# Kernel optimization log

Hardware: AMD Instinct MI355X
Metric: run time of the kernel (lower is better)

The kernel has to match this reference:

```python
import jax, jax.numpy as jnp
import numpy as np

B, N, F = 256, 32, 256
NUM_PASSING = 2


def _fc_edges(n):
    # all ordered pairs (send -> rec), i != j, matching NRI-style encode matrices
    send, rec = [], []
    for i in range(n):
        for j in range(n):
            if i != j:
                send.append(i)
                rec.append(j)
    return np.array(send, np.int32), np.array(rec, np.int32)


def setup_inputs() -> dict:
    key = jax.random.key(0)
    ks = jax.random.split(key, 16)
    send_np, rec_np = _fc_edges(N)

    def xavier(k, shape):
        fan_in, fan_out = shape
        std = (2.0 / (fan_in + fan_out)) ** 0.5
        return jax.random.normal(k, shape, jnp.float32) * std

    bias = lambda d: jnp.full((d,), 0.1, jnp.float32)
    return {
        "x": jax.random.normal(ks[0], (B, N, F), jnp.float32),
        "rec_idx": jnp.asarray(rec_np),
        "send_idx": jnp.asarray(send_np),
        "w_in1": xavier(ks[1], (F, 256)), "b_in1": bias(256),
        "w_in2": xavier(ks[2], (256, 256)), "b_in2": bias(256),
        "w_e1": xavier(ks[3], (512, 256)), "b_e1": bias(256),
        "w_e2": xavier(ks[4], (256, 256)), "b_e2": bias(256),
        "w_n1": xavier(ks[5], (256, 256)), "b_n1": bias(256),
        "w_n2": xavier(ks[6], (256, 256)), "b_n2": bias(256),
    }


def _mlp(h, wa, ba, wb, bb):
    # Linear -> ReLU -> (Dropout p=0) -> Linear -> ReLU
    return jax.nn.relu(jax.nn.relu(h @ wa + ba) @ wb + bb)


def reference(x, rec_idx, send_idx,
              w_in1, b_in1, w_in2, b_in2,
              w_e1, b_e1, w_e2, b_e2,
              w_n1, b_n1, w_n2, b_n2):
    n_nodes = x.shape[-2]
    # in-degree per node == rec_encode.sum(0)
    deg = jax.ops.segment_sum(jnp.ones_like(rec_idx, x.dtype), rec_idx,
                              num_segments=n_nodes)  # [N]
    h = _mlp(x, w_in1, b_in1, w_in2, b_in2)  # [B, N, 256]
    for _ in range(NUM_PASSING):
        # node2edge: gather (== one-hot matmul), cat [sends, recs]
        edges = jnp.concatenate([h[:, send_idx, :], h[:, rec_idx, :]], axis=-1)  # [B, E, 512]
        e = _mlp(edges, w_e1, b_e1, w_e2, b_e2)  # [B, E, 256]
        # edge2node: scatter-sum by receiver then divide by in-degree (mean)
        e_t = jnp.swapaxes(e, 0, 1)  # [E, B, 256]
        agg = jax.ops.segment_sum(e_t, rec_idx, num_segments=n_nodes)  # [N, B, 256]
        agg = jnp.swapaxes(agg, 0, 1) / deg[None, :, None]  # [B, N, 256]
        h = _mlp(agg, w_n1, b_n1, w_n2, b_n2)
    return h
```

## Files before the change

### kernel.cpp

```cpp
#include <hip/hip_runtime.h>


typedef short bf16x8 __attribute__((ext_vector_type(8)));
typedef float f32x4 __attribute__((ext_vector_type(4)));
typedef unsigned short ushort_t;

__device__ __forceinline__ unsigned short f2bf(float f) {
    unsigned u = __float_as_uint(f);
    u += 0x7fff + ((u >> 16) & 1);
    return (unsigned short)(u >> 16);
}
__device__ __forceinline__ float lo16f(unsigned w) { return __uint_as_float(w << 16); }
__device__ __forceinline__ float hi16f(unsigned w) { return __uint_as_float(w & 0xffff0000u); }
__device__ __forceinline__ unsigned cvt_pk_bf16(float lo, float hi) {
    unsigned r;
    asm volatile("v_cvt_pk_bf16_f32 %0, %1, %2" : "=v"(r) : "v"(lo), "v"(hi));
    return r;
}
__device__ __forceinline__ void gload16(const void* g, void* l) {
    __builtin_amdgcn_global_load_lds(
        (const __attribute__((address_space(1))) void*)g,
        (__attribute__((address_space(3))) void*)l, 16, 0, 0);
}

__global__ __launch_bounds__(256) void prep_weights(
    const float* __restrict__ w_in1, const float* __restrict__ w_in2,
    const float* __restrict__ w_e1,  const float* __restrict__ w_e2,
    const float* __restrict__ w_n1,  const float* __restrict__ w_n2,
    ushort_t* __restrict__ dst)
{
    __shared__ ushort_t tile[32][264];
    const int wid = blockIdx.x >> 3;
    const int kb  = blockIdx.x & 7;
    const float* src;
    switch (wid) {
        case 0: src = w_in1; break;
        case 1: src = w_in2; break;
        case 2: src = w_e1; break;
        case 3: src = w_e1 + 65536; break;
        case 4: src = w_e2; break;
        case 5: src = w_n1; break;
        default: src = w_n2; break;
    }
    const int t = threadIdx.x;
#pragma unroll
    for (int k0 = 0; k0 < 32; k0++)
        tile[k0][t] = f2bf(src[(size_t)(kb * 32 + k0) * 256 + t]);
    __syncthreads();
    ushort_t* base = dst + wid * 65536 + kb * 8192 + t * 32;
    const int sw = (t >> 1) & 3;
#pragma unroll
    for (int kc = 0; kc < 4; kc++) {
        union { uint4 q; ushort_t u[8]; } w;
#pragma unroll
        for (int ko = 0; ko < 8; ko++) w.u[ko] = tile[kc * 8 + ko][t];
        *(uint4*)&base[(kc ^ sw) * 8] = w.q;
    }
}

__global__ __launch_bounds__(256) void conv_x(
    const float* __restrict__ x, ushort_t* __restrict__ xb, int n8)
{
    int i = blockIdx.x * 256 + threadIdx.x;
    if (i >= n8) return;
    const float4* p = (const float4*)x + (size_t)i * 2;
    float4 a = p[0], b = p[1];
    ushort4 o0 = make_ushort4(f2bf(a.x), f2bf(a.y), f2bf(a.z), f2bf(a.w));
    ushort4 o1 = make_ushort4(f2bf(b.x), f2bf(b.y), f2bf(b.z), f2bf(b.w));
    ((ushort4*)xb)[(size_t)i * 2]     = o0;
    ((ushort4*)xb)[(size_t)i * 2 + 1] = o1;
}

template <int EPI>
__global__ __launch_bounds__(256) void gemm64(
    const ushort_t* __restrict__ A, const ushort_t* __restrict__ WB,
    const float* __restrict__ bias, void* __restrict__ out, int ldc, int split)
{
    __shared__ ushort_t As[2][2048];
    __shared__ ushort_t Bs[2][2048];

    const int mb = (blockIdx.x & 7) * 16 + (blockIdx.x >> 3);
    const int m0 = mb * 64;
    const int ny = blockIdx.y;
    int nloc; const ushort_t* wb; const float* bp; int nout;
    if (ny >= split) { nloc = (ny - split) * 64; wb = WB + 65536; bp = nullptr; nout = 256 + nloc; }
    else             { nloc = ny * 64;           wb = WB;         bp = bias;    nout = nloc; }

    const int t = threadIdx.x;
    const int lane = t & 63;
    const int w = t >> 6;
    const int wm = w >> 1, wn = w & 1;
    const int lr = lane & 15, lg = lane >> 4;

    const int arow = w * 16 + (lane >> 2);
    const int ac = (lane & 3) ^ ((arow >> 1) & 3);
    const ushort_t* asrc = A + (size_t)(m0 + arow) * 256 + ac * 8;
    const ushort_t* bsrc = wb + nloc * 32 + w * 512 + lane * 8;

    int aoff[2], boff[2];
#pragma unroll
    for (int f = 0; f < 2; f++) {
        int r = wm * 32 + f * 16 + lr;
        aoff[f] = r * 32 + ((lg ^ ((r >> 1) & 3)) * 8);
        int rb = wn * 32 + f * 16 + lr;
        boff[f] = rb * 32 + ((lg ^ ((rb >> 1) & 3)) * 8);
    }

    f32x4 acc[2][2] = {};

    gload16(asrc, &As[0][w * 512]);
    gload16(bsrc, &Bs[0][w * 512]);

    for (int kb = 1; kb < 8; kb++) {
        __syncthreads();
        gload16(asrc + kb * 32,   &As[kb & 1][w * 512]);
        gload16(bsrc + kb * 8192, &Bs[kb & 1][w * 512]);
        const int cur = (kb - 1) & 1;
        bf16x8 a0 = *(const bf16x8*)&As[cur][aoff[0]];
        bf16x8 a1 = *(const bf16x8*)&As[cur][aoff[1]];
        bf16x8 b0 = *(const bf16x8*)&Bs[cur][boff[0]];
        bf16x8 b1 = *(const bf16x8*)&Bs[cur][boff[1]];
        acc[0][0] = __builtin_amdgcn_mfma_f32_16x16x32_bf16(a0, b0, acc[0][0], 0, 0, 0);
        acc[0][1] = __builtin_amdgcn_mfma_f32_16x16x32_bf16(a0, b1, acc[0][1], 0, 0, 0);
        acc[1][0] = __builtin_amdgcn_mfma_f32_16x16x32_bf16(a1, b0, acc[1][0], 0, 0, 0);
        acc[1][1] = __builtin_amdgcn_mfma_f32_16x16x32_bf16(a1, b1, acc[1][1], 0, 0, 0);
    }
    __syncthreads();
    {
        bf16x8 a0 = *(const bf16x8*)&As[1][aoff[0]];
        bf16x8 a1 = *(const bf16x8*)&As[1][aoff[1]];
        bf16x8 b0 = *(const bf16x8*)&Bs[1][boff[0]];
        bf16x8 b1 = *(const bf16x8*)&Bs[1][boff[1]];
        acc[0][0] = __builtin_amdgcn_mfma_f32_16x16x32_bf16(a0, b0, acc[0][0], 0, 0, 0);
        acc[0][1] = __builtin_amdgcn_mfma_f32_16x16x32_bf16(a0, b1, acc[0][1], 0, 0, 0);
        acc[1][0] = __builtin_amdgcn_mfma_f32_16x16x32_bf16(a1, b0, acc[1][0], 0, 0, 0);
        acc[1][1] = __builtin_amdgcn_mfma_f32_16x16x32_bf16(a1, b1, acc[1][1], 0, 0, 0);
    }

#pragma unroll
    for (int fm = 0; fm < 2; fm++)
#pragma unroll
        for (int fn = 0; fn < 2; fn++) {
            const int cl = wn * 32 + fn * 16 + lr;
            float bv = 0.f;
            if (bp) bv = bp[nloc + cl];
#pragma unroll
            for (int r = 0; r < 4; r++) {
                const int row = m0 + wm * 32 + fm * 16 + lg * 4 + r;
                float v = acc[fm][fn][r] + bv;
                if constexpr (EPI == 2 || EPI == 3) v = fmaxf(v, 0.f);
                if constexpr (EPI == 3)
                    ((float*)out)[(size_t)row * ldc + nout + cl] = v;
                else
                    ((ushort_t*)out)[(size_t)row * ldc + nout + cl] = f2bf(v);
            }
        }
}

__global__ __launch_bounds__(256, 2) void edge_fused(
    const ushort_t* __restrict__ UVb,
    const ushort_t* __restrict__ WBsw,
    const float* __restrict__ b2,
    ushort_t* __restrict__ agg)
{
    __shared__ ushort_t As[2][4096];

    const int logical = (blockIdx.x & 7) * 256 + (blockIdx.x >> 3);
    const int bb = logical >> 3;
    const int g0 = (logical & 7) * 4;
    const int t = threadIdx.x;
    const int lane = t & 63;
    const int w = t >> 6;
    const int lr = lane & 15, lg = lane >> 4;

    const int brow = t >> 1;
    const int kh = t & 1;
    const int jr = brow >> 5;
    const int s = brow & 31;
    const int j = g0 + jr;
    const int si = (s == 31) ? j : (s + (s >= j ? 1 : 0));
    const ushort_t* up = UVb + (size_t)(bb * 32 + si) * 512 + kh * 16;
    const ushort_t* vp = UVb + (size_t)(bb * 32 + j) * 512 + 256 + kh * 16;
    const int swz = (brow >> 1) & 3;
    const int aw0 = brow * 32 + (((kh * 2)     ^ swz) * 8);
    const int aw1 = brow * 32 + (((kh * 2 + 1) ^ swz) * 8);

    int aoff[8];
#pragma unroll
    for (int m = 0; m < 8; m++) {
        const int r = m * 16 + lr;
        aoff[m] = r * 32 + ((lg ^ ((r >> 1) & 3)) * 8);
    }
    int boff[4];
#pragma unroll
    for (int fn = 0; fn < 4; fn++) {
        const int n = w * 64 + fn * 16 + lr;
        boff[fn] = n * 32 + ((lg ^ ((n >> 1) & 3)) * 8);
    }

    {
        uint4 ua = *(const uint4*)up,        ub = *(const uint4*)(up + 8);
        uint4 va = *(const uint4*)vp,        vb = *(const uint4*)(vp + 8);
        uint4 q0, q1;
        q0.x = cvt_pk_bf16(fmaxf(lo16f(ua.x) + lo16f(va.x), 0.f), fmaxf(hi16f(ua.x) + hi16f(va.x), 0.f));
        q0.y = cvt_pk_bf16(fmaxf(lo16f(ua.y) + lo16f(va.y), 0.f), fmaxf(hi16f(ua.y) + hi16f(va.y), 0.f));
        q0.z = cvt_pk_bf16(fmaxf(lo16f(ua.z) + lo16f(va.z), 0.f), fmaxf(hi16f(ua.z) + hi16f(va.z), 0.f));
        q0.w = cvt_pk_bf16(fmaxf(lo16f(ua.w) + lo16f(va.w), 0.f), fmaxf(hi16f(ua.w) + hi16f(va.w), 0.f));
        q1.x = cvt_pk_bf16(fmaxf(lo16f(ub.x) + lo16f(vb.x), 0.f), fmaxf(hi16f(ub.x) + hi16f(vb.x), 0.f));
        q1.y = cvt_pk_bf16(fmaxf(lo16f(ub.y) + lo16f(vb.y), 0.f), fmaxf(hi16f(ub.y) + hi16f(vb.y), 0.f));
        q1.z = cvt_pk_bf16(fmaxf(lo16f(ub.z) + lo16f(vb.z), 0.f), fmaxf(hi16f(ub.z) + hi16f(vb.z), 0.f));
        q1.w = cvt_pk_bf16(fmaxf(lo16f(ub.w) + lo16f(vb.w), 0.f), fmaxf(hi16f(ub.w) + hi16f(vb.w), 0.f));
        *(uint4*)&As[0][aw0] = q0;
        *(uint4*)&As[0][aw1] = q1;
    }
    bf16x8 bc[4];
#pragma unroll
    for (int fn = 0; fn < 4; fn++) bc[fn] = *(const bf16x8*)&WBsw[boff[fn]];

    f32x4 acc[8][4] = {};

#pragma unroll
    for (int kb = 0; kb < 8; kb++) {
        __syncthreads();
        uint4 ua, ub, va, vb;
        bf16x8 bn[4];
        if (kb < 7) {
            const ushort_t* upn = up + (kb + 1) * 32;
            const ushort_t* vpn = vp + (kb + 1) * 32;
            ua = *(const uint4*)upn;  ub = *(const uint4*)(upn + 8);
            va = *(const uint4*)vpn;  vb = *(const uint4*)(vpn + 8);
#pragma unroll
            for (int fn = 0; fn < 4; fn++)
                bn[fn] = *(const bf16x8*)&WBsw[(kb + 1) * 8192 + boff[fn]];
        }
        bf16x8 af[8];
#pragma unroll
        for (int m = 0; m < 8; m++) af[m] = *(const bf16x8*)&As[kb & 1][aoff[m]];
#pragma unroll
        for (int fn = 0; fn < 4; fn++)
#pragma unroll
            for (int m = 0; m < 8; m++)
                acc[m][fn] = __builtin_amdgcn_mfma_f32_16x16x32_bf16(
                    af[m], bc[fn], acc[m][fn], 0, 0, 0);
        if (kb < 7) {
            uint4 q0, q1;
            q0.x = cvt_pk_bf16(fmaxf(lo16f(ua.x) + lo16f(va.x), 0.f), fmaxf(hi16f(ua.x) + hi16f(va.x), 0.f));
            q0.y = cvt_pk_bf16(fmaxf(lo16f(ua.y) + lo16f(va.y), 0.f), fmaxf(hi16f(ua.y) + hi16f(va.y), 0.f));
            q0.z = cvt_pk_bf16(fmaxf(lo16f(ua.z) + lo16f(va.z), 0.f), fmaxf(hi16f(ua.z) + hi16f(va.z), 0.f));
            q0.w = cvt_pk_bf16(fmaxf(lo16f(ua.w) + lo16f(va.w), 0.f), fmaxf(hi16f(ua.w) + hi16f(va.w), 0.f));
            q1.x = cvt_pk_bf16(fmaxf(lo16f(ub.x) + lo16f(vb.x), 0.f), fmaxf(hi16f(ub.x) + hi16f(vb.x), 0.f));
            q1.y = cvt_pk_bf16(fmaxf(lo16f(ub.y) + lo16f(vb.y), 0.f), fmaxf(hi16f(ub.y) + hi16f(vb.y), 0.f));
            q1.z = cvt_pk_bf16(fmaxf(lo16f(ub.z) + lo16f(vb.z), 0.f), fmaxf(hi16f(ub.z) + hi16f(vb.z), 0.f));
            q1.w = cvt_pk_bf16(fmaxf(lo16f(ub.w) + lo16f(vb.w), 0.f), fmaxf(hi16f(ub.w) + hi16f(vb.w), 0.f));
            *(uint4*)&As[(kb + 1) & 1][aw0] = q0;
            *(uint4*)&As[(kb + 1) & 1][aw1] = q1;
#pragma unroll
            for (int fn = 0; fn < 4; fn++) bc[fn] = bn[fn];
        }
    }

#pragma unroll
    for (int fn = 0; fn < 4; fn++) {
        const int col = w * 64 + fn * 16 + lr;
        const float bvf = b2[col];
#pragma unroll
        for (int recv = 0; recv < 4; recv++) {
            float sum = 0.f;
#pragma unroll
            for (int q = 0; q < 2; q++) {
                const int fm = recv * 2 + q;
#pragma unroll
                for (int r = 0; r < 4; r++) {
                    float v = fmaxf(acc[fm][fn][r] + bvf, 0.f);
                    if (!(q == 1 && lg == 3 && r == 3)) sum += v;
                }
            }
            sum += __shfl_xor(sum, 16);
            sum += __shfl_xor(sum, 32);
            if (lane < 16)
                agg[(size_t)(bb * 32 + g0 + recv) * 256 + col] = f2bf(sum * (1.0f / 31.0f));
        }
    }
}

extern "C" void kernel_launch(void* const* d_in, const int* in_sizes, int n_in,
                              void* d_out, int out_size, void* d_ws, size_t ws_size,
                              hipStream_t stream)
{
    const float* x     = (const float*)d_in[0];
    const float* w_in1 = (const float*)d_in[3];
    const float* b_in1 = (const float*)d_in[4];
    const float* w_in2 = (const float*)d_in[5];
    const float* b_in2 = (const float*)d_in[6];
    const float* w_e1  = (const float*)d_in[7];
    const float* b_e1  = (const float*)d_in[8];
    const float* w_e2  = (const float*)d_in[9];
    const float* b_e2  = (const float*)d_in[10];
    const float* w_n1  = (const float*)d_in[11];
    const float* b_n1  = (const float*)d_in[12];
    const float* w_n2  = (const float*)d_in[13];
    const float* b_n2  = (const float*)d_in[14];

    char* ws = (char*)d_ws;
    size_t off = 0;
    auto alloc = [&](size_t n) { char* p = ws + off; off += (n + 255) & ~(size_t)255; return p; };

    ushort_t* wt  = (ushort_t*)alloc(7 * 65536 * sizeof(ushort_t));
    ushort_t* xb  = (ushort_t*)alloc(8192 * 256 * 2);
    ushort_t* h   = (ushort_t*)alloc(8192 * 256 * 2);
    ushort_t* t1  = (ushort_t*)alloc(8192 * 256 * 2);
    ushort_t* UVb = (ushort_t*)alloc(8192 * 512 * 2);
    ushort_t* ag  = (ushort_t*)alloc(8192 * 256 * 2);
    (void)ws_size; (void)in_sizes; (void)n_in; (void)out_size;

    prep_weights<<<56, 256, 0, stream>>>(w_in1, w_in2, w_e1, w_e2, w_n1, w_n2, wt);
    conv_x<<<1024, 256, 0, stream>>>(x, xb, 262144);

    dim3 gs(128, 4);
    gemm64<2><<<gs, 256, 0, stream>>>(xb, wt + 0 * 65536, b_in1, t1, 256, 99);
    gemm64<2><<<gs, 256, 0, stream>>>(t1, wt + 1 * 65536, b_in2, h, 256, 99);

    for (int p = 0; p < 2; p++) {
        dim3 guv(128, 8);
        gemm64<4><<<guv, 256, 0, stream>>>(h, wt + 2 * 65536, b_e1, UVb, 512, 4);
        edge_fused<<<2048, 256, 0, stream>>>(UVb, wt + 4 * 65536, b_e2, ag);
        gemm64<2><<<gs, 256, 0, stream>>>(ag, wt + 5 * 65536, b_n1, t1, 256, 99);
        if (p == 0)
            gemm64<2><<<gs, 256, 0, stream>>>(t1, wt + 6 * 65536, b_n2, h, 256, 99);
        else
            gemm64<3><<<gs, 256, 0, stream>>>(t1, wt + 6 * 65536, b_n2, (float*)d_out, 256, 99);
    }
}
```

Baseline: 146.4 us.

## Stage full-K A tiles in LDS and stream B from global in GEMMs

```diff
diff --git a/kernel.cpp b/kernel.cpp
--- a/kernel.cpp
+++ b/kernel.cpp
@@ -72,15 +72,14 @@
 }
 
 template <int EPI>
-__global__ __launch_bounds__(256) void gemm64(
+__global__ __launch_bounds__(256, 2) void gemm128(
     const ushort_t* __restrict__ A, const ushort_t* __restrict__ WB,
     const float* __restrict__ bias, void* __restrict__ out, int ldc, int split)
 {
-    __shared__ ushort_t As[2][2048];
-    __shared__ ushort_t Bs[2][2048];
-
-    const int mb = (blockIdx.x & 7) * 16 + (blockIdx.x >> 3);
-    const int m0 = mb * 64;
+    __shared__ ushort_t As[128 * 256];
+
+    const int mb = (blockIdx.x & 7) * 8 + (blockIdx.x >> 3);
+    const int m0 = mb * 128;
     const int ny = blockIdx.y;
     int nloc; const ushort_t* wb; const float* bp; int nout;
     if (ny >= split) { nloc = (ny - split) * 64; wb = WB + 65536; bp = nullptr; nout = 256 + nloc; }
@@ -89,70 +88,76 @@
     const int t = threadIdx.x;
     const int lane = t & 63;
     const int w = t >> 6;
-    const int wm = w >> 1, wn = w & 1;
     const int lr = lane & 15, lg = lane >> 4;
 
-    const int arow = w * 16 + (lane >> 2);
-    const int ac = (lane & 3) ^ ((arow >> 1) & 3);
-    const ushort_t* asrc = A + (size_t)(m0 + arow) * 256 + ac * 8;
-    const ushort_t* bsrc = wb + nloc * 32 + w * 512 + lane * 8;
-
-    int aoff[2], boff[2];
-#pragma unroll
-    for (int f = 0; f < 2; f++) {
-        int r = wm * 32 + f * 16 + lr;
-        aoff[f] = r * 32 + ((lg ^ ((r >> 1) & 3)) * 8);
-        int rb = wn * 32 + f * 16 + lr;
-        boff[f] = rb * 32 + ((lg ^ ((rb >> 1) & 3)) * 8);
-    }
-
-    f32x4 acc[2][2] = {};
-
-    gload16(asrc, &As[0][w * 512]);
-    gload16(bsrc, &Bs[0][w * 512]);
-
-    for (int kb = 1; kb < 8; kb++) {
-        __syncthreads();
-        gload16(asrc + kb * 32,   &As[kb & 1][w * 512]);
-        gload16(bsrc + kb * 8192, &Bs[kb & 1][w * 512]);
-        const int cur = (kb - 1) & 1;
-        bf16x8 a0 = *(const bf16x8*)&As[cur][aoff[0]];
-        bf16x8 a1 = *(const bf16x8*)&As[cur][aoff[1]];
-        bf16x8 b0 = *(const bf16x8*)&Bs[cur][boff[0]];
-        bf16x8 b1 = *(const bf16x8*)&Bs[cur][boff[1]];
-        acc[0][0] = __builtin_amdgcn_mfma_f32_16x16x32_bf16(a0, b0, acc[0][0], 0, 0, 0);
-        acc[0][1] = __builtin_amdgcn_mfma_f32_16x16x32_bf16(a0, b1, acc[0][1], 0, 0, 0);
-        acc[1][0] = __builtin_amdgcn_mfma_f32_16x16x32_bf16(a1, b0, acc[1][0], 0, 0, 0);
-        acc[1][1] = __builtin_amdgcn_mfma_f32_16x16x32_bf16(a1, b1, acc[1][1], 0, 0, 0);
-    }
+    {
+        const int r0  = w * 2 + (lane >> 5);
+        const int kcp = lane & 31;
+        const ushort_t* src = A + (size_t)(m0 + r0) * 256 + ((kcp ^ (r0 & 7)) * 8);
+        ushort_t* dst = &As[w * 512];
+#pragma unroll
+        for (int i = 0; i < 16; i++)
+            gload16(src + i * 2048, dst + i * 2048);
+    }
+
+    int boffs[4]; float bv[4];
+#pragma unroll
+    for (int fn = 0; fn < 4; fn++) {
+        const int n = nloc + fn * 16 + lr;
+        boffs[fn] = n * 32 + ((lg ^ ((n >> 1) & 3)) * 8);
+        bv[fn] = bp ? bp[n] : 0.f;
+    }
+    int abase[2], asw[2];
+#pragma unroll
+    for (int fm = 0; fm < 2; fm++) {
+        const int r = w * 32 + fm * 16 + lr;
+        abase[fm] = r * 256;
+        asw[fm] = r & 7;
+    }
+
+    bf16x8 bc[4];
+#pragma unroll
+    for (int fn = 0; fn < 4; fn++) bc[fn] = *(const bf16x8*)&wb[boffs[fn]];
+
     __syncthreads();
-    {
-        bf16x8 a0 = *(const bf16x8*)&As[1][aoff[0]];
-        bf16x8 a1 = *(const bf16x8*)&As[1][aoff[1]];
-        bf16x8 b0 = *(const bf16x8*)&Bs[1][boff[0]];
-        bf16x8 b1 = *(const bf16x8*)&Bs[1][boff[1]];
-        acc[0][0] = __builtin_amdgcn_mfma_f32_16x16x32_bf16(a0, b0, acc[0][0], 0, 0, 0);
-        acc[0][1] = __builtin_amdgcn_mfma_f32_16x16x32_bf16(a0, b1, acc[0][1], 0, 0, 0);
-        acc[1][0] = __builtin_amdgcn_mfma_f32_16x16x32_bf16(a1, b0, acc[1][0], 0, 0, 0);
-        acc[1][1] = __builtin_amdgcn_mfma_f32_16x16x32_bf16(a1, b1, acc[1][1], 0, 0, 0);
+
+    f32x4 acc[2][4] = {};
+#pragma unroll
+    for (int kb = 0; kb < 8; kb++) {
+        bf16x8 bn[4];
+        if (kb < 7)
+#pragma unroll
+            for (int fn = 0; fn < 4; fn++)
+                bn[fn] = *(const bf16x8*)&wb[(kb + 1) * 8192 + boffs[fn]];
+        bf16x8 af[2];
+#pragma unroll
+        for (int fm = 0; fm < 2; fm++)
+            af[fm] = *(const bf16x8*)&As[abase[fm] + (((kb * 4 + lg) ^ asw[fm]) * 8)];
+#pragma unroll
+        for (int fm = 0; fm < 2; fm++)
+#pragma unroll
+            for (int fn = 0; fn < 4; fn++)
+                acc[fm][fn] = __builtin_amdgcn_mfma_f32_16x16x32_bf16(
+                    af[fm], bc[fn], acc[fm][fn], 0, 0, 0);
+        if (kb < 7)
+#pragma unroll
+            for (int fn = 0; fn < 4; fn++) bc[fn] = bn[fn];
     }
 
 #pragma unroll
     for (int fm = 0; fm < 2; fm++)
 #pragma unroll
-        for (int fn = 0; fn < 2; fn++) {
-            const int cl = wn * 32 + fn * 16 + lr;
-            float bv = 0.f;
-            if (bp) bv = bp[nloc + cl];
+        for (int fn = 0; fn < 4; fn++) {
+            const int col = nout + fn * 16 + lr;
 #pragma unroll
             for (int r = 0; r < 4; r++) {
-                const int row = m0 + wm * 32 + fm * 16 + lg * 4 + r;
-                float v = acc[fm][fn][r] + bv;
+                const int row = m0 + w * 32 + fm * 16 + lg * 4 + r;
+                float v = acc[fm][fn][r] + bv[fn];
                 if constexpr (EPI == 2 || EPI == 3) v = fmaxf(v, 0.f);
                 if constexpr (EPI == 3)
-                    ((float*)out)[(size_t)row * ldc + nout + cl] = v;
+                    ((float*)out)[(size_t)row * ldc + col] = v;
                 else
-                    ((ushort_t*)out)[(size_t)row * ldc + nout + cl] = f2bf(v);
+                    ((ushort_t*)out)[(size_t)row * ldc + col] = f2bf(v);
             }
         }
 }
@@ -163,7 +168,7 @@
     const float* __restrict__ b2,
     ushort_t* __restrict__ agg)
 {
-    __shared__ ushort_t As[2][4096];
+    __shared__ ushort_t As[128 * 256];
 
     const int logical = (blockIdx.x & 7) * 256 + (blockIdx.x >> 3);
     const int bb = logical >> 3;
@@ -173,96 +178,77 @@
     const int w = t >> 6;
     const int lr = lane & 15, lg = lane >> 4;
 
-    const int brow = t >> 1;
-    const int kh = t & 1;
-    const int jr = brow >> 5;
-    const int s = brow & 31;
-    const int j = g0 + jr;
+    const int br = t >> 1;
+    const int h  = t & 1;
+    const int jr = br >> 5;
+    const int s  = br & 31;
+    const int j  = g0 + jr;
     const int si = (s == 31) ? j : (s + (s >= j ? 1 : 0));
-    const ushort_t* up = UVb + (size_t)(bb * 32 + si) * 512 + kh * 16;
-    const ushort_t* vp = UVb + (size_t)(bb * 32 + j) * 512 + 256 + kh * 16;
-    const int swz = (brow >> 1) & 3;
-    const int aw0 = brow * 32 + (((kh * 2)     ^ swz) * 8);
-    const int aw1 = brow * 32 + (((kh * 2 + 1) ^ swz) * 8);
-
-    int aoff[8];
+    const ushort_t* up = UVb + (size_t)(bb * 32 + si) * 512 + h * 128;
+    const ushort_t* vp = UVb + (size_t)(bb * 32 + j) * 512 + 256 + h * 128;
+    ushort_t* aw = &As[br * 256];
+    const int bsw = br & 7;
+
+#pragma unroll
+    for (int i = 0; i < 16; i++) {
+        uint4 u = *(const uint4*)(up + i * 8);
+        uint4 v = *(const uint4*)(vp + i * 8);
+        uint4 q;
+        q.x = cvt_pk_bf16(fmaxf(lo16f(u.x) + lo16f(v.x), 0.f), fmaxf(hi16f(u.x) + hi16f(v.x), 0.f));
+        q.y = cvt_pk_bf16(fmaxf(lo16f(u.y) + lo16f(v.y), 0.f), fmaxf(hi16f(u.y) + hi16f(v.y), 0.f));
+        q.z = cvt_pk_bf16(fmaxf(lo16f(u.z) + lo16f(v.z), 0.f), fmaxf(hi16f(u.z) + hi16f(v.z), 0.f));
+        q.w = cvt_pk_bf16(fmaxf(lo16f(u.w) + lo16f(v.w), 0.f), fmaxf(hi16f(u.w) + hi16f(v.w), 0.f));
+        *(uint4*)&aw[((h * 16 + i) ^ bsw) * 8] = q;
+    }
+
+    int abase[8], asw[8];
 #pragma unroll
     for (int m = 0; m < 8; m++) {
         const int r = m * 16 + lr;
-        aoff[m] = r * 32 + ((lg ^ ((r >> 1) & 3)) * 8);
-    }
-    int boff[4];
+        abase[m] = r * 256;
+        asw[m] = r & 7;
+    }
+    int boffs[4]; float bv[4];
 #pragma unroll
     for (int fn = 0; fn < 4; fn++) {
         const int n = w * 64 + fn * 16 + lr;
-        boff[fn] = n * 32 + ((lg ^ ((n >> 1) & 3)) * 8);
-    }
-
-    {
-        uint4 ua = *(const uint4*)up,        ub = *(const uint4*)(up + 8);
-        uint4 va = *(const uint4*)vp,        vb = *(const uint4*)(vp + 8);
-        uint4 q0, q1;
-        q0.x = cvt_pk_bf16(fmaxf(lo16f(ua.x) + lo16f(va.x), 0.f), fmaxf(hi16f(ua.x) + hi16f(va.x), 0.f));
-        q0.y = cvt_pk_bf16(fmaxf(lo16f(ua.y) + lo16f(va.y), 0.f), fmaxf(hi16f(ua.y) + hi16f(va.y), 0.f));
-        q0.z = cvt_pk_bf16(fmaxf(lo16f(ua.z) + lo16f(va.z), 0.f), fmaxf(hi16f(ua.z) + hi16f(va.z), 0.f));
-        q0.w = cvt_pk_bf16(fmaxf(lo16f(ua.w) + lo16f(va.w), 0.f), fmaxf(hi16f(ua.w) + hi16f(va.w), 0.f));
-        q1.x = cvt_pk_bf16(fmaxf(lo16f(ub.x) + lo16f(vb.x), 0.f), fmaxf(hi16f(ub.x) + hi16f(vb.x), 0.f));
-        q1.y = cvt_pk_bf16(fmaxf(lo16f(ub.y) + lo16f(vb.y), 0.f), fmaxf(hi16f(ub.y) + hi16f(vb.y), 0.f));
-        q1.z = cvt_pk_bf16(fmaxf(lo16f(ub.z) + lo16f(vb.z), 0.f), fmaxf(hi16f(ub.z) + hi16f(vb.z), 0.f));
-        q1.w = cvt_pk_bf16(fmaxf(lo16f(ub.w) + lo16f(vb.w), 0.f), fmaxf(hi16f(ub.w) + hi16f(vb.w), 0.f));
-        *(uint4*)&As[0][aw0] = q0;
-        *(uint4*)&As[0][aw1] = q1;
+        boffs[fn] = n * 32 + ((lg ^ ((n >> 1) & 3)) * 8);
+        bv[fn] = b2[n];
     }
     bf16x8 bc[4];
 #pragma unroll
-    for (int fn = 0; fn < 4; fn++) bc[fn] = *(const bf16x8*)&WBsw[boff[fn]];
+    for (int fn = 0; fn < 4; fn++) bc[fn] = *(const bf16x8*)&WBsw[boffs[fn]];
+
+    __syncthreads();
 
     f32x4 acc[8][4] = {};
-
 #pragma unroll
     for (int kb = 0; kb < 8; kb++) {
-        __syncthreads();
-        uint4 ua, ub, va, vb;
         bf16x8 bn[4];
-        if (kb < 7) {
-            const ushort_t* upn = up + (kb + 1) * 32;
-            const ushort_t* vpn = vp + (kb + 1) * 32;
-            ua = *(const uint4*)upn;  ub = *(const uint4*)(upn + 8);
-            va = *(const uint4*)vpn;  vb = *(const uint4*)(vpn + 8);
+        if (kb < 7)
 #pragma unroll
             for (int fn = 0; fn < 4; fn++)
-                bn[fn] = *(const bf16x8*)&WBsw[(kb + 1) * 8192 + boff[fn]];
-        }
+                bn[fn] = *(const bf16x8*)&WBsw[(kb + 1) * 8192 + boffs[fn]];
         bf16x8 af[8];
 #pragma unroll
-        for (int m = 0; m < 8; m++) af[m] = *(const bf16x8*)&As[kb & 1][aoff[m]];
+        for (int m = 0; m < 8; m++)
+            af[m] = *(const bf16x8*)&As[abase[m] + (((kb * 4 + lg) ^ asw[m]) * 8)];
+        __builtin_amdgcn_s_setprio(1);
 #pragma unroll
         for (int fn = 0; fn < 4; fn++)
 #pragma unroll
             for (int m = 0; m < 8; m++)
                 acc[m][fn] = __builtin_amdgcn_mfma_f32_16x16x32_bf16(
                     af[m], bc[fn], acc[m][fn], 0, 0, 0);
-        if (kb < 7) {
-            uint4 q0, q1;
-            q0.x = cvt_pk_bf16(fmaxf(lo16f(ua.x) + lo16f(va.x), 0.f), fmaxf(hi16f(ua.x) + hi16f(va.x), 0.f));
-            q0.y = cvt_pk_bf16(fmaxf(lo16f(ua.y) + lo16f(va.y), 0.f), fmaxf(hi16f(ua.y) + hi16f(va.y), 0.f));
-            q0.z = cvt_pk_bf16(fmaxf(lo16f(ua.z) + lo16f(va.z), 0.f), fmaxf(hi16f(ua.z) + hi16f(va.z), 0.f));
-            q0.w = cvt_pk_bf16(fmaxf(lo16f(ua.w) + lo16f(va.w), 0.f), fmaxf(hi16f(ua.w) + hi16f(va.w), 0.f));
-            q1.x = cvt_pk_bf16(fmaxf(lo16f(ub.x) + lo16f(vb.x), 0.f), fmaxf(hi16f(ub.x) + hi16f(vb.x), 0.f));
-            q1.y = cvt_pk_bf16(fmaxf(lo16f(ub.y) + lo16f(vb.y), 0.f), fmaxf(hi16f(ub.y) + hi16f(vb.y), 0.f));
-            q1.z = cvt_pk_bf16(fmaxf(lo16f(ub.z) + lo16f(vb.z), 0.f), fmaxf(hi16f(ub.z) + hi16f(vb.z), 0.f));
-            q1.w = cvt_pk_bf16(fmaxf(lo16f(ub.w) + lo16f(vb.w), 0.f), fmaxf(hi16f(ub.w) + hi16f(vb.w), 0.f));
-            *(uint4*)&As[(kb + 1) & 1][aw0] = q0;
-            *(uint4*)&As[(kb + 1) & 1][aw1] = q1;
+        __builtin_amdgcn_s_setprio(0);
+        if (kb < 7)
 #pragma unroll
             for (int fn = 0; fn < 4; fn++) bc[fn] = bn[fn];
-        }
     }
 
 #pragma unroll
     for (int fn = 0; fn < 4; fn++) {
         const int col = w * 64 + fn * 16 + lr;
-        const float bvf = b2[col];
 #pragma unroll
         for (int recv = 0; recv < 4; recv++) {
             float sum = 0.f;
@@ -271,7 +257,7 @@
                 const int fm = recv * 2 + q;
 #pragma unroll
                 for (int r = 0; r < 4; r++) {
-                    float v = fmaxf(acc[fm][fn][r] + bvf, 0.f);
+                    float v = fmaxf(acc[fm][fn][r] + bv[fn], 0.f);
                     if (!(q == 1 && lg == 3 && r == 3)) sum += v;
                 }
             }
@@ -316,18 +302,18 @@
     prep_weights<<<56, 256, 0, stream>>>(w_in1, w_in2, w_e1, w_e2, w_n1, w_n2, wt);
     conv_x<<<1024, 256, 0, stream>>>(x, xb, 262144);
 
-    dim3 gs(128, 4);
-    gemm64<2><<<gs, 256, 0, stream>>>(xb, wt + 0 * 65536, b_in1, t1, 256, 99);
-    gemm64<2><<<gs, 256, 0, stream>>>(t1, wt + 1 * 65536, b_in2, h, 256, 99);
+    dim3 gs(64, 4);
+    gemm128<2><<<gs, 256, 0, stream>>>(xb, wt + 0 * 65536, b_in1, t1, 256, 99);
+    gemm128<2><<<gs, 256, 0, stream>>>(t1, wt + 1 * 65536, b_in2, h, 256, 99);
 
     for (int p = 0; p < 2; p++) {
-        dim3 guv(128, 8);
-        gemm64<4><<<guv, 256, 0, stream>>>(h, wt + 2 * 65536, b_e1, UVb, 512, 4);
+        dim3 guv(64, 8);
+        gemm128<4><<<guv, 256, 0, stream>>>(h, wt + 2 * 65536, b_e1, UVb, 512, 4);
         edge_fused<<<2048, 256, 0, stream>>>(UVb, wt + 4 * 65536, b_e2, ag);
-        gemm64<2><<<gs, 256, 0, stream>>>(ag, wt + 5 * 65536, b_n1, t1, 256, 99);
+        gemm128<2><<<gs, 256, 0, stream>>>(ag, wt + 5 * 65536, b_n1, t1, 256, 99);
         if (p == 0)
-            gemm64<2><<<gs, 256, 0, stream>>>(t1, wt + 6 * 65536, b_n2, h, 256, 99);
+            gemm128<2><<<gs, 256, 0, stream>>>(t1, wt + 6 * 65536, b_n2, h, 256, 99);
         else
-            gemm64<3><<<gs, 256, 0, stream>>>(t1, wt + 6 * 65536, b_n2, (float*)d_out, 256, 99);
-    }
-}
+            gemm128<3><<<gs, 256, 0, stream>>>(t1, wt + 6 * 65536, b_n2, (float*)d_out, 256, 99);
+    }
+}
```

Result: slower. 156.5 us (+6.9%).

## Fuse chained node MLP GEMMs into one LDS-resident kernel per row block

Applied to the files above, without the earlier changes.

```diff
diff --git a/kernel.cpp b/kernel.cpp
--- a/kernel.cpp
+++ b/kernel.cpp
@@ -71,90 +71,208 @@
     ((ushort4*)xb)[(size_t)i * 2 + 1] = o1;
 }
 
-template <int EPI>
-__global__ __launch_bounds__(256) void gemm64(
-    const ushort_t* __restrict__ A, const ushort_t* __restrict__ WB,
-    const float* __restrict__ bias, void* __restrict__ out, int ldc, int split)
-{
-    __shared__ ushort_t As[2][2048];
-    __shared__ ushort_t Bs[2][2048];
-
-    const int mb = (blockIdx.x & 7) * 16 + (blockIdx.x >> 3);
-    const int m0 = mb * 64;
-    const int ny = blockIdx.y;
-    int nloc; const ushort_t* wb; const float* bp; int nout;
-    if (ny >= split) { nloc = (ny - split) * 64; wb = WB + 65536; bp = nullptr; nout = 256 + nloc; }
-    else             { nloc = ny * 64;           wb = WB;         bp = bias;    nout = nloc; }
-
+
+__device__ __forceinline__ void layer_to_lds(
+    const ushort_t* __restrict__ wimg, const float* __restrict__ bias,
+    const ushort_t* __restrict__ As, ushort_t* __restrict__ Ad,
+    const int w, const int lr, const int lg)
+{
+    int boffs[4]; float4 b4[4];
+#pragma unroll
+    for (int fn = 0; fn < 4; fn++) {
+        const int n = w * 64 + fn * 16 + lr;
+        boffs[fn] = n * 32 + ((lg ^ ((n >> 1) & 3)) * 8);
+        b4[fn] = *(const float4*)&bias[w * 64 + fn * 16 + lg * 4];
+    }
+    bf16x8 bc[4];
+#pragma unroll
+    for (int fn = 0; fn < 4; fn++) bc[fn] = *(const bf16x8*)&wimg[boffs[fn]];
+    f32x4 acc[4][2] = {};
+#pragma unroll
+    for (int kb = 0; kb < 8; kb++) {
+        bf16x8 bn[4];
+        if (kb < 7)
+#pragma unroll
+            for (int fn = 0; fn < 4; fn++)
+                bn[fn] = *(const bf16x8*)&wimg[(kb + 1) * 8192 + boffs[fn]];
+        bf16x8 af[2];
+#pragma unroll
+        for (int fm = 0; fm < 2; fm++) {
+            const int r = fm * 16 + lr;
+            af[fm] = *(const bf16x8*)&As[r * 256 + (((kb * 4 + lg) ^ (r & 7)) * 8)];
+        }
+#pragma unroll
+        for (int fn = 0; fn < 4; fn++)
+#pragma unroll
+            for (int fm = 0; fm < 2; fm++)
+                acc[fn][fm] = __builtin_amdgcn_mfma_f32_16x16x32_bf16(
+                    bc[fn], af[fm], acc[fn][fm], 0, 0, 0);
+        if (kb < 7)
+#pragma unroll
+            for (int fn = 0; fn < 4; fn++) bc[fn] = bn[fn];
+    }
+#pragma unroll
+    for (int fn = 0; fn < 4; fn++) {
+        const int k0 = w * 64 + fn * 16 + lg * 4;
+        const int kc = k0 >> 3, kj = k0 & 7;
+#pragma unroll
+        for (int fm = 0; fm < 2; fm++) {
+            const int m = fm * 16 + lr;
+            float v0 = fmaxf(acc[fn][fm][0] + b4[fn].x, 0.f);
+            float v1 = fmaxf(acc[fn][fm][1] + b4[fn].y, 0.f);
+            float v2 = fmaxf(acc[fn][fm][2] + b4[fn].z, 0.f);
+            float v3 = fmaxf(acc[fn][fm][3] + b4[fn].w, 0.f);
+            uint2 q = { cvt_pk_bf16(v0, v1), cvt_pk_bf16(v2, v3) };
+            *(uint2*)&Ad[m * 256 + ((kc ^ (m & 7)) * 8) + kj] = q;
+        }
+    }
+}
+
+__device__ __forceinline__ void layer_e1(
+    const ushort_t* __restrict__ wE, const float* __restrict__ bE,
+    const ushort_t* __restrict__ As, ushort_t* __restrict__ UVb,
+    const int m0, const int w, const int lr, const int lg)
+{
+    const ushort_t* wimg = (w < 2) ? wE : (wE + 65536);
+    const int nb = (w & 1) * 128;
+    int boffs[8]; float4 b4[8];
+#pragma unroll
+    for (int fn = 0; fn < 8; fn++) {
+        const int n = nb + fn * 16 + lr;
+        boffs[fn] = n * 32 + ((lg ^ ((n >> 1) & 3)) * 8);
+        if (w < 2) b4[fn] = *(const float4*)&bE[nb + fn * 16 + lg * 4];
+        else       b4[fn] = make_float4(0.f, 0.f, 0.f, 0.f);
+    }
+    bf16x8 bc[8];
+#pragma unroll
+    for (int fn = 0; fn < 8; fn++) bc[fn] = *(const bf16x8*)&wimg[boffs[fn]];
+    f32x4 acc[8][2] = {};
+#pragma unroll
+    for (int kb = 0; kb < 8; kb++) {
+        bf16x8 bn[8];
+        if (kb < 7)
+#pragma unroll
+            for (int fn = 0; fn < 8; fn++)
+                bn[fn] = *(const bf16x8*)&wimg[(kb + 1) * 8192 + boffs[fn]];
+        bf16x8 af[2];
+#pragma unroll
+        for (int fm = 0; fm < 2; fm++) {
+            const int r = fm * 16 + lr;
+            af[fm] = *(const bf16x8*)&As[r * 256 + (((kb * 4 + lg) ^ (r & 7)) * 8)];
+        }
+#pragma unroll
+        for (int fn = 0; fn < 8; fn++)
+#pragma unroll
+            for (int fm = 0; fm < 2; fm++)
+                acc[fn][fm] = __builtin_amdgcn_mfma_f32_16x16x32_bf16(
+                    bc[fn], af[fm], acc[fn][fm], 0, 0, 0);
+        if (kb < 7)
+#pragma unroll
+            for (int fn = 0; fn < 8; fn++) bc[fn] = bn[fn];
+    }
+#pragma unroll
+    for (int fn = 0; fn < 8; fn++) {
+        const int nglob = w * 128 + fn * 16 + lg * 4;
+#pragma unroll
+        for (int fm = 0; fm < 2; fm++) {
+            const int node = m0 + fm * 16 + lr;
+            float v0 = acc[fn][fm][0] + b4[fn].x;
+            float v1 = acc[fn][fm][1] + b4[fn].y;
+            float v2 = acc[fn][fm][2] + b4[fn].z;
+            float v3 = acc[fn][fm][3] + b4[fn].w;
+            uint2 q = { cvt_pk_bf16(v0, v1), cvt_pk_bf16(v2, v3) };
+            *(uint2*)&UVb[(size_t)node * 512 + nglob] = q;
+        }
+    }
+}
+
+__device__ __forceinline__ void layer_fin(
+    const ushort_t* __restrict__ wimg, const float* __restrict__ bias,
+    const ushort_t* __restrict__ As, float* __restrict__ out,
+    const int m0, const int w, const int lr, const int lg)
+{
+    int boffs[4]; float4 b4[4];
+#pragma unroll
+    for (int fn = 0; fn < 4; fn++) {
+        const int n = w * 64 + fn * 16 + lr;
+        boffs[fn] = n * 32 + ((lg ^ ((n >> 1) & 3)) * 8);
+        b4[fn] = *(const float4*)&bias[w * 64 + fn * 16 + lg * 4];
+    }
+    bf16x8 bc[4];
+#pragma unroll
+    for (int fn = 0; fn < 4; fn++) bc[fn] = *(const bf16x8*)&wimg[boffs[fn]];
+    f32x4 acc[4][2] = {};
+#pragma unroll
+    for (int kb = 0; kb < 8; kb++) {
+        bf16x8 bn[4];
+        if (kb < 7)
+#pragma unroll
+            for (int fn = 0; fn < 4; fn++)
+                bn[fn] = *(const bf16x8*)&wimg[(kb + 1) * 8192 + boffs[fn]];
+        bf16x8 af[2];
+#pragma unroll
+        for (int fm = 0; fm < 2; fm++) {
+            const int r = fm * 16 + lr;
+            af[fm] = *(const bf16x8*)&As[r * 256 + (((kb * 4 + lg) ^ (r & 7)) * 8)];
+        }
+#pragma unroll
+        for (int fn = 0; fn < 4; fn++)
+#pragma unroll
+            for (int fm = 0; fm < 2; fm++)
+                acc[fn][fm] = __builtin_amdgcn_mfma_f32_16x16x32_bf16(
+                    bc[fn], af[fm], acc[fn][fm], 0, 0, 0);
+        if (kb < 7)
+#pragma unroll
+            for (int fn = 0; fn < 4; fn++) bc[fn] = bn[fn];
+    }
+#pragma unroll
+    for (int fn = 0; fn < 4; fn++) {
+        const int col = w * 64 + fn * 16 + lg * 4;
+#pragma unroll
+        for (int fm = 0; fm < 2; fm++) {
+            const int row = m0 + fm * 16 + lr;
+            float4 o;
+            o.x = fmaxf(acc[fn][fm][0] + b4[fn].x, 0.f);
+            o.y = fmaxf(acc[fn][fm][1] + b4[fn].y, 0.f);
+            o.z = fmaxf(acc[fn][fm][2] + b4[fn].z, 0.f);
+            o.w = fmaxf(acc[fn][fm][3] + b4[fn].w, 0.f);
+            *(float4*)&out[(size_t)row * 256 + col] = o;
+        }
+    }
+}
+
+template <int THREE>
+__global__ __launch_bounds__(256, 2) void mlp_chain(
+    const ushort_t* __restrict__ in,
+    const ushort_t* __restrict__ wA, const float* __restrict__ bA,
+    const ushort_t* __restrict__ wB, const float* __restrict__ bB,
+    const ushort_t* __restrict__ wE, const float* __restrict__ bE,
+    void* __restrict__ out)
+{
+    __shared__ ushort_t A0[32 * 256];
+    __shared__ ushort_t A1[32 * 256];
+    const int m0 = blockIdx.x * 32;
     const int t = threadIdx.x;
-    const int lane = t & 63;
-    const int w = t >> 6;
-    const int wm = w >> 1, wn = w & 1;
+    const int lane = t & 63, w = t >> 6;
     const int lr = lane & 15, lg = lane >> 4;
 
-    const int arow = w * 16 + (lane >> 2);
-    const int ac = (lane & 3) ^ ((arow >> 1) & 3);
-    const ushort_t* asrc = A + (size_t)(m0 + arow) * 256 + ac * 8;
-    const ushort_t* bsrc = wb + nloc * 32 + w * 512 + lane * 8;
-
-    int aoff[2], boff[2];
-#pragma unroll
-    for (int f = 0; f < 2; f++) {
-        int r = wm * 32 + f * 16 + lr;
-        aoff[f] = r * 32 + ((lg ^ ((r >> 1) & 3)) * 8);
-        int rb = wn * 32 + f * 16 + lr;
-        boff[f] = rb * 32 + ((lg ^ ((rb >> 1) & 3)) * 8);
-    }
-
-    f32x4 acc[2][2] = {};
-
-    gload16(asrc, &As[0][w * 512]);
-    gload16(bsrc, &Bs[0][w * 512]);
-
-    for (int kb = 1; kb < 8; kb++) {
+#pragma unroll
+    for (int i = 0; i < 4; i++) {
+        const int r = i * 8 + (t >> 5);
+        const int p = t & 31;
+        gload16(in + (size_t)(m0 + r) * 256 + ((p ^ (r & 7)) * 8), &A0[i * 2048 + t * 8]);
+    }
+    __syncthreads();
+
+    layer_to_lds(wA, bA, A0, A1, w, lr, lg);
+    __syncthreads();
+    if constexpr (THREE) {
+        layer_to_lds(wB, bB, A1, A0, w, lr, lg);
         __syncthreads();
-        gload16(asrc + kb * 32,   &As[kb & 1][w * 512]);
-        gload16(bsrc + kb * 8192, &Bs[kb & 1][w * 512]);
-        const int cur = (kb - 1) & 1;
-        bf16x8 a0 = *(const bf16x8*)&As[cur][aoff[0]];
-        bf16x8 a1 = *(const bf16x8*)&As[cur][aoff[1]];
-        bf16x8 b0 = *(const bf16x8*)&Bs[cur][boff[0]];
-        bf16x8 b1 = *(const bf16x8*)&Bs[cur][boff[1]];
-        acc[0][0] = __builtin_amdgcn_mfma_f32_16x16x32_bf16(a0, b0, acc[0][0], 0, 0, 0);
-        acc[0][1] = __builtin_amdgcn_mfma_f32_16x16x32_bf16(a0, b1, acc[0][1], 0, 0, 0);
-        acc[1][0] = __builtin_amdgcn_mfma_f32_16x16x32_bf16(a1, b0, acc[1][0], 0, 0, 0);
-        acc[1][1] = __builtin_amdgcn_mfma_f32_16x16x32_bf16(a1, b1, acc[1][1], 0, 0, 0);
-    }
-    __syncthreads();
-    {
-        bf16x8 a0 = *(const bf16x8*)&As[1][aoff[0]];
-        bf16x8 a1 = *(const bf16x8*)&As[1][aoff[1]];
-        bf16x8 b0 = *(const bf16x8*)&Bs[1][boff[0]];
-        bf16x8 b1 = *(const bf16x8*)&Bs[1][boff[1]];
-        acc[0][0] = __builtin_amdgcn_mfma_f32_16x16x32_bf16(a0, b0, acc[0][0], 0, 0, 0);
-        acc[0][1] = __builtin_amdgcn_mfma_f32_16x16x32_bf16(a0, b1, acc[0][1], 0, 0, 0);
-        acc[1][0] = __builtin_amdgcn_mfma_f32_16x16x32_bf16(a1, b0, acc[1][0], 0, 0, 0);
-        acc[1][1] = __builtin_amdgcn_mfma_f32_16x16x32_bf16(a1, b1, acc[1][1], 0, 0, 0);
-    }
-
-#pragma unroll
-    for (int fm = 0; fm < 2; fm++)
-#pragma unroll
-        for (int fn = 0; fn < 2; fn++) {
-            const int cl = wn * 32 + fn * 16 + lr;
-            float bv = 0.f;
-            if (bp) bv = bp[nloc + cl];
-#pragma unroll
-            for (int r = 0; r < 4; r++) {
-                const int row = m0 + wm * 32 + fm * 16 + lg * 4 + r;
-                float v = acc[fm][fn][r] + bv;
-                if constexpr (EPI == 2 || EPI == 3) v = fmaxf(v, 0.f);
-                if constexpr (EPI == 3)
-                    ((float*)out)[(size_t)row * ldc + nout + cl] = v;
-                else
-                    ((ushort_t*)out)[(size_t)row * ldc + nout + cl] = f2bf(v);
-            }
-        }
+        layer_e1(wE, bE, A0, (ushort_t*)out, m0, w, lr, lg);
+    } else {
+        layer_fin(wB, bB, A1, (float*)out, m0, w, lr, lg);
+    }
 }
 
 __global__ __launch_bounds__(256, 2) void edge_fused(
@@ -236,12 +354,14 @@
         bf16x8 af[8];
 #pragma unroll
         for (int m = 0; m < 8; m++) af[m] = *(const bf16x8*)&As[kb & 1][aoff[m]];
+        __builtin_amdgcn_s_setprio(1);
 #pragma unroll
         for (int fn = 0; fn < 4; fn++)
 #pragma unroll
             for (int m = 0; m < 8; m++)
                 acc[m][fn] = __builtin_amdgcn_mfma_f32_16x16x32_bf16(
                     af[m], bc[fn], acc[m][fn], 0, 0, 0);
+        __builtin_amdgcn_s_setprio(0);
         if (kb < 7) {
             uint4 q0, q1;
             q0.x = cvt_pk_bf16(fmaxf(lo16f(ua.x) + lo16f(va.x), 0.f), fmaxf(hi16f(ua.x) + hi16f(va.x), 0.f));
@@ -307,8 +427,6 @@
 
     ushort_t* wt  = (ushort_t*)alloc(7 * 65536 * sizeof(ushort_t));
     ushort_t* xb  = (ushort_t*)alloc(8192 * 256 * 2);
-    ushort_t* h   = (ushort_t*)alloc(8192 * 256 * 2);
-    ushort_t* t1  = (ushort_t*)alloc(8192 * 256 * 2);
     ushort_t* UVb = (ushort_t*)alloc(8192 * 512 * 2);
     ushort_t* ag  = (ushort_t*)alloc(8192 * 256 * 2);
     (void)ws_size; (void)in_sizes; (void)n_in; (void)out_size;
@@ -316,18 +434,12 @@
     prep_weights<<<56, 256, 0, stream>>>(w_in1, w_in2, w_e1, w_e2, w_n1, w_n2, wt);
     conv_x<<<1024, 256, 0, stream>>>(x, xb, 262144);
 
-    dim3 gs(128, 4);
-    gemm64<2><<<gs, 256, 0, stream>>>(xb, wt + 0 * 65536, b_in1, t1, 256, 99);
-    gemm64<2><<<gs, 256, 0, stream>>>(t1, wt + 1 * 65536, b_in2, h, 256, 99);
-
-    for (int p = 0; p < 2; p++) {
-        dim3 guv(128, 8);
-        gemm64<4><<<guv, 256, 0, stream>>>(h, wt + 2 * 65536, b_e1, UVb, 512, 4);
-        edge_fused<<<2048, 256, 0, stream>>>(UVb, wt + 4 * 65536, b_e2, ag);
-        gemm64<2><<<gs, 256, 0, stream>>>(ag, wt + 5 * 65536, b_n1, t1, 256, 99);
-        if (p == 0)
-            gemm64<2><<<gs, 256, 0, stream>>>(t1, wt + 6 * 65536, b_n2, h, 256, 99);
-        else
-            gemm64<3><<<gs, 256, 0, stream>>>(t1, wt + 6 * 65536, b_n2, (float*)d_out, 256, 99);
-    }
-}
+    mlp_chain<1><<<256, 256, 0, stream>>>(xb,
+        wt + 0 * 65536, b_in1, wt + 1 * 65536, b_in2, wt + 2 * 65536, b_e1, UVb);
+    edge_fused<<<2048, 256, 0, stream>>>(UVb, wt + 4 * 65536, b_e2, ag);
+    mlp_chain<1><<<256, 256, 0, stream>>>(ag,
+        wt + 5 * 65536, b_n1, wt + 6 * 65536, b_n2, wt + 2 * 65536, b_e1, UVb);
+    edge_fused<<<2048, 256, 0, stream>>>(UVb, wt + 4 * 65536, b_e2, ag);
+    mlp_chain<0><<<256, 256, 0, stream>>>(ag,
+        wt + 5 * 65536, b_n1, wt + 6 * 65536, b_n2, nullptr, nullptr, d_out);
+}
```

After: 135.6 us. -7.4%, faster.
